# Kernel optimization log

Measured on AMD Instinct MI355X. Metric: run time of the kernel, lower is better.

The kernel has to match this reference:

```python
import jax, jax.numpy as jnp
import numpy as np

N = 50000      # nodes
E = 800000     # edges (before self-loops)
F = 128        # num_features
H = 64         # hidden_channels
B = 512        # batch_size (num graphs)
NC = 10        # num_classes


def setup_inputs() -> dict:
    key = jax.random.key(0)
    ks = jax.random.split(key, 24)
    rn = lambda k, shp, s=0.05: jax.random.normal(k, shp, jnp.float32) * s
    inp = {}
    inp["x"] = jax.random.normal(ks[0], (N, F), jnp.float32)
    inp["edge_index"] = jax.random.randint(ks[1], (2, E), 0, N)
    inp["batch"] = jnp.sort(jax.random.randint(ks[2], (N,), 0, B))
    # GATConv1: in F -> 4 heads x H (concat)
    inp["W1"] = rn(ks[3], (F, 4 * H)); inp["a_src1"] = rn(ks[4], (4, H))
    inp["a_dst1"] = rn(ks[5], (4, H)); inp["b1"] = rn(ks[6], (4 * H,))
    # GATConv2: in 4H -> 1 head x 2H
    inp["W2"] = rn(ks[7], (4 * H, 2 * H)); inp["a_src2"] = rn(ks[8], (1, 2 * H))
    inp["a_dst2"] = rn(ks[9], (1, 2 * H)); inp["b2"] = rn(ks[10], (2 * H,))
    # GCNConv: in 2H -> H
    inp["Wg"] = rn(ks[11], (2 * H, H)); inp["bg"] = rn(ks[12], (H,))
    # BatchNorms (eval mode: running_mean=0, running_var=1)
    inp["bn1_g"] = 1.0 + rn(ks[13], (4 * H,)); inp["bn1_b"] = rn(ks[14], (4 * H,))
    inp["bn2_g"] = 1.0 + rn(ks[15], (2 * H,)); inp["bn2_b"] = rn(ks[16], (2 * H,))
    inp["bn3_g"] = 1.0 + rn(ks[17], (2 * H,)); inp["bn3_b"] = rn(ks[18], (2 * H,))
    inp["lin1_W"] = rn(ks[19], (H, 128)); inp["lin1_b"] = rn(ks[20], (128,))
    inp["lin2_W"] = rn(ks[21], (128, NC)); inp["lin2_b"] = rn(ks[22], (NC,))
    inp["batch_size"] = B
    return inp


def _gat(x, src, dst, W, a_s, a_d, b, n):
    """PyG GATConv (eval): project, edge attention (leaky_relu 0.2), dst-softmax, scatter."""
    heads, ch = a_s.shape
    h = (x @ W).reshape(n, heads, ch)                       # [N, heads, ch]
    sc_s = (h * a_s).sum(-1)                                # [N, heads]
    sc_d = (h * a_d).sum(-1)
    e = jax.nn.leaky_relu(sc_s[src] + sc_d[dst], 0.2)       # [E2, heads]
    m = jax.ops.segment_max(e, dst, num_segments=n)
    ee = jnp.exp(e - m[dst])
    s = jax.ops.segment_sum(ee, dst, num_segments=n)
    alpha = ee / (s[dst] + 1e-16)                           # edge softmax per dst
    out = jax.ops.segment_sum(h[src] * alpha[:, :, None], dst, num_segments=n)
    return out.reshape(n, heads * ch) + b


def _bn_eval(x, g, b, eps=1e-5):
    # BatchNorm1d eval with running_mean=0, running_var=1
    return x * (g / jnp.sqrt(1.0 + eps)) + b


def reference(x, edge_index, batch, W1, a_src1, a_dst1, b1, W2, a_src2, a_dst2, b2,
              Wg, bg, bn1_g, bn1_b, bn2_g, bn2_b, bn3_g, bn3_b,
              lin1_W, lin1_b, lin2_W, lin2_b, batch_size):
    n = x.shape[0]
    loop = jnp.arange(n)
    src = jnp.concatenate([edge_index[0], loop])            # add self-loops (PyG default)
    dst = jnp.concatenate([edge_index[1], loop])
    lrelu = lambda v: jax.nn.leaky_relu(v, 0.01)            # module's LeakyReLU()

    x1 = _bn_eval(lrelu(_gat(x, src, dst, W1, a_src1, a_dst1, b1, n)), bn1_g, bn1_b)
    x2 = _bn_eval(lrelu(_gat(x1, src, dst, W2, a_src2, a_dst2, b2, n)), bn2_g, bn2_b)

    # GCNConv with symmetric normalization over A + I
    deg = jax.ops.segment_sum(jnp.ones_like(dst, jnp.float32), dst, num_segments=n)
    dis = jnp.where(deg > 0, jax.lax.rsqrt(deg), 0.0)
    h = x2 @ Wg                                             # [N, H]
    msg = h[src] * (dis[src] * dis[dst])[:, None]
    x3 = lrelu(jax.ops.segment_sum(msg, dst, num_segments=n) + bg)

    # global_mean_pool over graphs (dropout is identity in eval)
    sums = jax.ops.segment_sum(x3, batch, num_segments=batch_size)
    cnt = jax.ops.segment_sum(jnp.ones((n,), jnp.float32), batch, num_segments=batch_size)
    pooled = sums / jnp.clip(cnt, 1.0)[:, None]             # [B, H]

    y = lrelu(_bn_eval(pooled @ lin1_W + lin1_b, bn3_g, bn3_b))
    return y @ lin2_W + lin2_b                              # [B, NC]
```

## Files before the change

kernel.cpp:

```cpp
#include <hip/hip_runtime.h>
#include <hip/hip_bf16.h>

#define NN  50000
#define EE  800000
#define NE2 850000
#define NB  512
#define NRT 3125
#define NSB 196

#define BN_RS 0.9999950000374997f

typedef __attribute__((ext_vector_type(8))) short short8;
typedef __attribute__((ext_vector_type(4))) float f32x4;

__device__ __forceinline__ float bf2f(__hip_bfloat16 v) { return __bfloat162float(v); }
__device__ __forceinline__ unsigned short f2b(float v) {
    __hip_bfloat16 b = __float2bfloat16(v);
    return *reinterpret_cast<unsigned short*>(&b);
}
__device__ __forceinline__ float u2f(unsigned short u) {
    union { unsigned u; float f; } c; c.u = ((unsigned)u) << 16; return c.f;
}
__device__ __forceinline__ float4 u42f4(ushort4 v) {
    float4 r; r.x = u2f(v.x); r.y = u2f(v.y); r.z = u2f(v.z); r.w = u2f(v.w); return r;
}
__device__ __forceinline__ float lrelu01(float v) { return v > 0.f ? v : 0.01f * v; }
__device__ __forceinline__ float lrelu02(float v) { return v > 0.f ? v : 0.2f * v; }

__device__ __forceinline__ void up2(unsigned u, float& lo, float& hi) {
    union { unsigned x; float f; } a, b;
    a.x = u << 16; b.x = u & 0xFFFF0000u;
    lo = a.f; hi = b.f;
}
__device__ __forceinline__ void acc8(float* acc, uint4 u, float e) {
    float lo, hi;
    up2(u.x, lo, hi); acc[0] = fmaf(lo, e, acc[0]); acc[1] = fmaf(hi, e, acc[1]);
    up2(u.y, lo, hi); acc[2] = fmaf(lo, e, acc[2]); acc[3] = fmaf(hi, e, acc[3]);
    up2(u.z, lo, hi); acc[4] = fmaf(lo, e, acc[4]); acc[5] = fmaf(hi, e, acc[5]);
    up2(u.w, lo, hi); acc[6] = fmaf(lo, e, acc[6]); acc[7] = fmaf(hi, e, acc[7]);
}
__device__ __forceinline__ unsigned packbf2(float lo, float hi) {
    return ((unsigned)f2b(hi) << 16) | (unsigned)f2b(lo);
}

__device__ __forceinline__ void edge_sd(const int* __restrict__ ei, int e, int& s, int& d) {
    if (e < EE) { s = ei[e]; d = ei[EE + e]; }
    else        { s = e - EE; d = e - EE; }
}

__device__ __forceinline__ float ldf(const void* p, int i, bool bf) {
    return bf ? bf2f(((const __hip_bfloat16*)p)[i]) : ((const float*)p)[i];
}

#define NSEG 20
#define WTOT 85578
#define XQUADS (NN * 32)
#define PREP_TOT (XQUADS + WTOT + 32768 + 32768 + 8192 + NE2)
struct SegArgs { const void* src[NSEG]; int off[NSEG]; };

__global__ __launch_bounds__(256) void prep_k(SegArgs a,
                                              const void* __restrict__ x_raw,
                                              ushort4* __restrict__ xb4,
                                              const void* __restrict__ W1r,
                                              const void* __restrict__ W2r,
                                              const void* __restrict__ Wgr,
                                              float* __restrict__ wf,
                                              unsigned short* __restrict__ W1t,
                                              unsigned short* __restrict__ W2t,
                                              unsigned short* __restrict__ Wgt,
                                              const int* __restrict__ ei,
                                              int* __restrict__ degi,
                                              int* __restrict__ flag) {
    __shared__ int cnt;
    int t = threadIdx.x;
    if (t == 0) cnt = 0;
    __syncthreads();
    {
        int c = 0;
        const unsigned* xw = (const unsigned*)x_raw;
#pragma unroll
        for (int k = 0; k < 4; ++k) {
            unsigned w = xw[t * 4 + k];
            unsigned ef = (w >> 7) & 0xFFu;
            if (ef >= 100u && ef <= 140u) c++;
        }
        atomicAdd(&cnt, c);
    }
    __syncthreads();
    bool bf = (cnt > 512);
    if (blockIdx.x == 0 && t == 0) *flag = bf ? 1 : 0;

    int i = blockIdx.x * 256 + t;
    if (i >= PREP_TOT) return;
    if (i < XQUADS) {
        ushort4 o;
        if (bf) o = ((const ushort4*)x_raw)[i];
        else {
            float4 v = ((const float4*)x_raw)[i];
            o.x = f2b(v.x); o.y = f2b(v.y); o.z = f2b(v.z); o.w = f2b(v.w);
        }
        xb4[i] = o;
        return;
    }
    i -= XQUADS;
    if (i < WTOT) {
        int s = 0;
#pragma unroll
        for (int k = 1; k < NSEG; ++k) if (i >= a.off[k]) s = k;
        wf[i] = ldf(a.src[s], i - a.off[s], bf);
        return;
    }
    i -= WTOT;
    if (i < 32768) {
        int n = i >> 7, k = i & 127;
        W1t[i] = f2b(ldf(W1r, k * 256 + n, bf));
        return;
    }
    i -= 32768;
    if (i < 32768) {
        int n = i >> 8, k = i & 255;
        W2t[i] = f2b(ldf(W2r, k * 128 + n, bf));
        return;
    }
    i -= 32768;
    if (i < 8192) {
        int n = i >> 7, k = i & 127;
        Wgt[i] = f2b(ldf(Wgr, k * 64 + n, bf));
        return;
    }
    i -= 8192;
    {
        int s, d; edge_sd(ei, i, s, d);
        atomicAdd(&degi[d], 1);
    }
}

__global__ __launch_bounds__(256) void pscan_k(const int* __restrict__ degi,
                                               int* __restrict__ incl, int* __restrict__ bsum) {
    __shared__ int tmp[256];
    int t = threadIdx.x;
    int i = blockIdx.x * 256 + t;
    int v = (i < NN) ? degi[i] : 0;
    tmp[t] = v;
    __syncthreads();
#pragma unroll
    for (int off = 1; off < 256; off <<= 1) {
        int u = (t >= off) ? tmp[t - off] : 0;
        __syncthreads();
        tmp[t] += u;
        __syncthreads();
    }
    if (i < NN) incl[i] = tmp[t];
    if (t == 255) bsum[blockIdx.x] = tmp[255];
}

__global__ __launch_bounds__(256) void bscan_k(int* __restrict__ bsum) {
    __shared__ int tmp[256];
    int t = threadIdx.x;
    tmp[t] = (t < NSB) ? bsum[t] : 0;
    __syncthreads();
#pragma unroll
    for (int off = 1; off < 256; off <<= 1) {
        int u = (t >= off) ? tmp[t - off] : 0;
        __syncthreads();
        tmp[t] += u;
        __syncthreads();
    }
    if (t < NSB) bsum[t] = tmp[t];
}

__global__ __launch_bounds__(256) void fscan_k(const int* __restrict__ degi,
                                               const int* __restrict__ incl,
                                               const int* __restrict__ bsum,
                                               const int* __restrict__ batch,
                                               int* __restrict__ row_ptr, int* __restrict__ cursor,
                                               float* __restrict__ dis, int* __restrict__ gstart) {
    int i = blockIdx.x * 256 + threadIdx.x;
    if (i <= NB) {
        int lo = 0, hi = NN;
        while (lo < hi) { int mid = (lo + hi) >> 1; if (batch[mid] < i) lo = mid + 1; else hi = mid; }
        gstart[i] = lo;
    }
    if (i >= NN) return;
    int dg = degi[i];
    int base = (blockIdx.x > 0) ? bsum[blockIdx.x - 1] : 0;
    int ex = base + incl[i] - dg;
    row_ptr[i] = ex; cursor[i] = ex;
    dis[i] = dg > 0 ? rsqrtf((float)dg) : 0.f;
    if (i == NN - 1) row_ptr[NN] = bsum[NSB - 1];
}

__global__ __launch_bounds__(256) void scatter_k(const int* __restrict__ ei,
                                                 int* __restrict__ cursor,
                                                 int* __restrict__ csr_src) {
    int e = blockIdx.x * 256 + threadIdx.x;
    if (e >= NE2) return;
    int s, d; edge_sd(ei, e, s, d);
    int pos = atomicAdd(&cursor[d], 1);
    csr_src[pos] = s;
}

__global__ __launch_bounds__(256) void mgemm1_k(const short* __restrict__ A,
                                                const short* __restrict__ Bt,
                                                unsigned short* __restrict__ C,
                                                const float* __restrict__ a_s,
                                                const float* __restrict__ a_d,
                                                float* __restrict__ sc_s,
                                                float* __restrict__ sc_d) {
    int wave = threadIdx.x >> 6, lane = threadIdx.x & 63;
    int rt = blockIdx.x, cg = wave;
    int l15 = lane & 15, quad = lane >> 4;
    const short* ap = A + (size_t)(rt * 16 + l15) * 128 + quad * 8;
    const short* bp = Bt + (size_t)(cg * 64 + l15) * 128 + quad * 8;
    f32x4 acc[4] = {};
    for (int k0 = 0; k0 < 128; k0 += 32) {
        short8 a = *(const short8*)(ap + k0);
#pragma unroll
        for (int j = 0; j < 4; ++j) {
            short8 b = *(const short8*)(bp + (size_t)j * 16 * 128 + k0);
            acc[j] = __builtin_amdgcn_mfma_f32_16x16x32_bf16(a, b, acc[j], 0, 0, 0);
        }
    }
    float asv[4], adv[4];
#pragma unroll
    for (int j = 0; j < 4; ++j) {
        asv[j] = a_s[cg * 64 + j * 16 + l15];
        adv[j] = a_d[cg * 64 + j * 16 + l15];
    }
    float ss[4] = {0.f, 0.f, 0.f, 0.f}, sd[4] = {0.f, 0.f, 0.f, 0.f};
#pragma unroll
    for (int j = 0; j < 4; ++j) {
        int n = cg * 64 + j * 16 + l15;
#pragma unroll
        for (int r = 0; r < 4; ++r) {
            float v = acc[j][r];
            C[(size_t)(rt * 16 + quad * 4 + r) * 256 + n] = f2b(v);
            ss[r] = fmaf(v, asv[j], ss[r]);
            sd[r] = fmaf(v, adv[j], sd[r]);
        }
    }
#pragma unroll
    for (int off = 1; off < 16; off <<= 1) {
#pragma unroll
        for (int r = 0; r < 4; ++r) {
            ss[r] += __shfl_xor(ss[r], off);
            sd[r] += __shfl_xor(sd[r], off);
        }
    }
    if (l15 == 0) {
#pragma unroll
        for (int r = 0; r < 4; ++r) {
            int node = rt * 16 + quad * 4 + r;
            sc_s[node * 4 + cg] = ss[r];
            sc_d[node * 4 + cg] = sd[r];
        }
    }
}

__global__ __launch_bounds__(256) void mgemm2_k(const short* __restrict__ A,
                                                const short* __restrict__ Bt,
                                                unsigned short* __restrict__ C,
                                                const float* __restrict__ a_s,
                                                const float* __restrict__ a_d,
                                                float* __restrict__ sc_s,
                                                float* __restrict__ sc_d) {
    __shared__ float sred[4][16][2];
    int wave = threadIdx.x >> 6, lane = threadIdx.x & 63;
    int gidx = blockIdx.x * 4 + wave;
    bool act = gidx < NRT * 2;
    int gcl = act ? gidx : NRT * 2 - 1;
    int rt = gcl >> 1, cg = gcl & 1;
    int l15 = lane & 15, quad = lane >> 4;
    const short* ap = A + (size_t)(rt * 16 + l15) * 256 + quad * 8;
    const short* bp = Bt + (size_t)(cg * 64 + l15) * 256 + quad * 8;
    f32x4 acc[4] = {};
    for (int k0 = 0; k0 < 256; k0 += 32) {
        short8 a = *(const short8*)(ap + k0);
#pragma unroll
        for (int j = 0; j < 4; ++j) {
            short8 b = *(const short8*)(bp + (size_t)j * 16 * 256 + k0);
            acc[j] = __builtin_amdgcn_mfma_f32_16x16x32_bf16(a, b, acc[j], 0, 0, 0);
        }
    }
    float asv[4], adv[4];
#pragma unroll
    for (int j = 0; j < 4; ++j) {
        asv[j] = a_s[cg * 64 + j * 16 + l15];
        adv[j] = a_d[cg * 64 + j * 16 + l15];
    }
    float ss[4] = {0.f, 0.f, 0.f, 0.f}, sd[4] = {0.f, 0.f, 0.f, 0.f};
#pragma unroll
    for (int j = 0; j < 4; ++j) {
        int n = cg * 64 + j * 16 + l15;
#pragma unroll
        for (int r = 0; r < 4; ++r) {
            float v = acc[j][r];
            if (act) C[(size_t)(rt * 16 + quad * 4 + r) * 128 + n] = f2b(v);
            ss[r] = fmaf(v, asv[j], ss[r]);
            sd[r] = fmaf(v, adv[j], sd[r]);
        }
    }
#pragma unroll
    for (int off = 1; off < 16; off <<= 1) {
#pragma unroll
        for (int r = 0; r < 4; ++r) {
            ss[r] += __shfl_xor(ss[r], off);
            sd[r] += __shfl_xor(sd[r], off);
        }
    }
    if (l15 == 0) {
#pragma unroll
        for (int r = 0; r < 4; ++r) {
            sred[wave][quad * 4 + r][0] = ss[r];
            sred[wave][quad * 4 + r][1] = sd[r];
        }
    }
    __syncthreads();
    if (threadIdx.x < 32) {
        int rl = threadIdx.x >> 4, row = threadIdx.x & 15;
        int g2 = blockIdx.x * 4 + rl * 2;
        if (g2 < NRT * 2) {
            int node = (g2 >> 1) * 16 + row;
            sc_s[node] = sred[rl * 2][row][0] + sred[rl * 2 + 1][row][0];
            sc_d[node] = sred[rl * 2][row][1] + sred[rl * 2 + 1][row][1];
        }
    }
}

__global__ __launch_bounds__(256) void mgemm3_k(const short* __restrict__ A,
                                                const short* __restrict__ Bt,
                                                unsigned short* __restrict__ C) {
    int wave = threadIdx.x >> 6, lane = threadIdx.x & 63;
    int gidx = blockIdx.x * 4 + wave;
    if (gidx >= NRT) return;
    int rt = gidx;
    int l15 = lane & 15, quad = lane >> 4;
    const short* ap = A + (size_t)(rt * 16 + l15) * 128 + quad * 8;
    const short* bp = Bt + (size_t)l15 * 128 + quad * 8;
    f32x4 acc[4] = {};
    for (int k0 = 0; k0 < 128; k0 += 32) {
        short8 a = *(const short8*)(ap + k0);
#pragma unroll
        for (int j = 0; j < 4; ++j) {
            short8 b = *(const short8*)(bp + (size_t)j * 16 * 128 + k0);
            acc[j] = __builtin_amdgcn_mfma_f32_16x16x32_bf16(a, b, acc[j], 0, 0, 0);
        }
    }
#pragma unroll
    for (int j = 0; j < 4; ++j) {
        int n = j * 16 + l15;
#pragma unroll
        for (int r = 0; r < 4; ++r)
            C[(size_t)(rt * 16 + quad * 4 + r) * 64 + n] = f2b(acc[j][r]);
    }
}

__device__ __forceinline__ float sel4(float4 v, int head) {
    float ab = (head & 1) ? v.y : v.x;
    float cd = (head & 1) ? v.w : v.z;
    return (head & 2) ? cd : ab;
}

__global__ __launch_bounds__(256) void agg1_k(const int* __restrict__ row_ptr,
                                              const int* __restrict__ csr_src,
                                              const uint4* __restrict__ h1b,
                                              const float4* __restrict__ sc_s4,
                                              const float4* __restrict__ sc_d4,
                                              const float4* __restrict__ b1,
                                              const float4* __restrict__ g1,
                                              const float4* __restrict__ bb1,
                                              uint4* __restrict__ x1b) {
    int n = __builtin_amdgcn_readfirstlane((blockIdx.x * 256 + threadIdx.x) >> 6);
    int lane = threadIdx.x & 63;
    if (n >= NN) return;
    int g = lane >> 5, sl = lane & 31;
    int head = sl >> 3;
    int row = row_ptr[n], end = row_ptr[n + 1];
    float scd_h = sel4(sc_d4[n], head);
    float acc[8] = {0.f, 0.f, 0.f, 0.f, 0.f, 0.f, 0.f, 0.f};
    float den = 0.f;
    int c = row + g;
    for (; c + 6 < end; c += 8) {
        int s0 = csr_src[c], s1 = csr_src[c + 2], s2 = csr_src[c + 4], s3 = csr_src[c + 6];
        float4 q0 = sc_s4[s0], q1 = sc_s4[s1], q2 = sc_s4[s2], q3 = sc_s4[s3];
        uint4 u0 = h1b[(size_t)s0 * 32 + sl];
        uint4 u1 = h1b[(size_t)s1 * 32 + sl];
        uint4 u2 = h1b[(size_t)s2 * 32 + sl];
        uint4 u3 = h1b[(size_t)s3 * 32 + sl];
        float e0 = __expf(lrelu02(sel4(q0, head) + scd_h));
        float e1 = __expf(lrelu02(sel4(q1, head) + scd_h));
        float e2 = __expf(lrelu02(sel4(q2, head) + scd_h));
        float e3 = __expf(lrelu02(sel4(q3, head) + scd_h));
        den += (e0 + e1) + (e2 + e3);
        acc8(acc, u0, e0); acc8(acc, u1, e1); acc8(acc, u2, e2); acc8(acc, u3, e3);
    }
    for (; c < end; c += 2) {
        int s0 = csr_src[c];
        float4 q0 = sc_s4[s0];
        uint4 u0 = h1b[(size_t)s0 * 32 + sl];
        float e0 = __expf(lrelu02(sel4(q0, head) + scd_h));
        den += e0;
        acc8(acc, u0, e0);
    }
    den += __shfl_xor(den, 32);
#pragma unroll
    for (int k = 0; k < 8; ++k) acc[k] += __shfl_xor(acc[k], 32);
    if (g == 0) {
        float inv = 1.f / (den + 1e-16f);
        float4 bA = b1[sl * 2],  bB = b1[sl * 2 + 1];
        float4 gA = g1[sl * 2],  gB = g1[sl * 2 + 1];
        float4 eA = bb1[sl * 2], eB = bb1[sl * 2 + 1];
        float o0 = lrelu01(fmaf(acc[0], inv, bA.x)) * (gA.x * BN_RS) + eA.x;
        float o1 = lrelu01(fmaf(acc[1], inv, bA.y)) * (gA.y * BN_RS) + eA.y;
        float o2 = lrelu01(fmaf(acc[2], inv, bA.z)) * (gA.z * BN_RS) + eA.z;
        float o3 = lrelu01(fmaf(acc[3], inv, bA.w)) * (gA.w * BN_RS) + eA.w;
        float o4 = lrelu01(fmaf(acc[4], inv, bB.x)) * (gB.x * BN_RS) + eB.x;
        float o5 = lrelu01(fmaf(acc[5], inv, bB.y)) * (gB.y * BN_RS) + eB.y;
        float o6 = lrelu01(fmaf(acc[6], inv, bB.z)) * (gB.z * BN_RS) + eB.z;
        float o7 = lrelu01(fmaf(acc[7], inv, bB.w)) * (gB.w * BN_RS) + eB.w;
        uint4 w;
        w.x = packbf2(o0, o1); w.y = packbf2(o2, o3);
        w.z = packbf2(o4, o5); w.w = packbf2(o6, o7);
        x1b[(size_t)n * 32 + sl] = w;
    }
}

__global__ __launch_bounds__(256) void agg2_k(const int* __restrict__ row_ptr,
                                              const int* __restrict__ csr_src,
                                              const uint4* __restrict__ h2b,
                                              const float* __restrict__ sc_s,
                                              const float* __restrict__ sc_d,
                                              const float4* __restrict__ b2,
                                              const float4* __restrict__ g2,
                                              const float4* __restrict__ bb2,
                                              uint4* __restrict__ x2b) {
    int n = __builtin_amdgcn_readfirstlane((blockIdx.x * 256 + threadIdx.x) >> 6);
    int lane = threadIdx.x & 63;
    if (n >= NN) return;
    int g = lane >> 4, sl = lane & 15;
    int row = row_ptr[n], end = row_ptr[n + 1];
    float scd = sc_d[n];
    float acc[8] = {0.f, 0.f, 0.f, 0.f, 0.f, 0.f, 0.f, 0.f};
    float den = 0.f;
    int c = row + g;
    for (; c + 12 < end; c += 16) {
        int s0 = csr_src[c], s1 = csr_src[c + 4], s2 = csr_src[c + 8], s3 = csr_src[c + 12];
        float c0 = sc_s[s0], c1 = sc_s[s1], c2 = sc_s[s2], c3 = sc_s[s3];
        uint4 u0 = h2b[(size_t)s0 * 16 + sl];
        uint4 u1 = h2b[(size_t)s1 * 16 + sl];
        uint4 u2 = h2b[(size_t)s2 * 16 + sl];
        uint4 u3 = h2b[(size_t)s3 * 16 + sl];
        float e0 = __expf(lrelu02(c0 + scd));
        float e1 = __expf(lrelu02(c1 + scd));
        float e2 = __expf(lrelu02(c2 + scd));
        float e3 = __expf(lrelu02(c3 + scd));
        den += (e0 + e1) + (e2 + e3);
        acc8(acc, u0, e0); acc8(acc, u1, e1); acc8(acc, u2, e2); acc8(acc, u3, e3);
    }
    for (; c < end; c += 4) {
        int s0 = csr_src[c];
        float e0 = __expf(lrelu02(sc_s[s0] + scd));
        uint4 u0 = h2b[(size_t)s0 * 16 + sl];
        den += e0;
        acc8(acc, u0, e0);
    }
    den += __shfl_xor(den, 16);
    den += __shfl_xor(den, 32);
#pragma unroll
    for (int k = 0; k < 8; ++k) {
        acc[k] += __shfl_xor(acc[k], 16);
        acc[k] += __shfl_xor(acc[k], 32);
    }
    if (lane < 16) {
        float inv = 1.f / (den + 1e-16f);
        float4 bA = b2[sl * 2],  bB = b2[sl * 2 + 1];
        float4 gA = g2[sl * 2],  gB = g2[sl * 2 + 1];
        float4 eA = bb2[sl * 2], eB = bb2[sl * 2 + 1];
        float o0 = lrelu01(fmaf(acc[0], inv, bA.x)) * (gA.x * BN_RS) + eA.x;
        float o1 = lrelu01(fmaf(acc[1], inv, bA.y)) * (gA.y * BN_RS) + eA.y;
        float o2 = lrelu01(fmaf(acc[2], inv, bA.z)) * (gA.z * BN_RS) + eA.z;
        float o3 = lrelu01(fmaf(acc[3], inv, bA.w)) * (gA.w * BN_RS) + eA.w;
        float o4 = lrelu01(fmaf(acc[4], inv, bB.x)) * (gB.x * BN_RS) + eB.x;
        float o5 = lrelu01(fmaf(acc[5], inv, bB.y)) * (gB.y * BN_RS) + eB.y;
        float o6 = lrelu01(fmaf(acc[6], inv, bB.z)) * (gB.z * BN_RS) + eB.z;
        float o7 = lrelu01(fmaf(acc[7], inv, bB.w)) * (gB.w * BN_RS) + eB.w;
        uint4 w;
        w.x = packbf2(o0, o1); w.y = packbf2(o2, o3);
        w.z = packbf2(o4, o5); w.w = packbf2(o6, o7);
        x2b[(size_t)n * 16 + sl] = w;
    }
}

__global__ __launch_bounds__(256) void gcn_k(const int* __restrict__ row_ptr,
                                             const int* __restrict__ csr_src,
                                             const uint4* __restrict__ hgb,
                                             const float* __restrict__ dis,
                                             const float4* __restrict__ bg,
                                             float4* __restrict__ x3) {
    int n = __builtin_amdgcn_readfirstlane((blockIdx.x * 256 + threadIdx.x) >> 6);
    int lane = threadIdx.x & 63;
    if (n >= NN) return;
    int g = lane >> 3, sl = lane & 7;
    int row = row_ptr[n], end = row_ptr[n + 1];
    float dn = dis[n];
    float acc[8] = {0.f, 0.f, 0.f, 0.f, 0.f, 0.f, 0.f, 0.f};
    int c = row + g;
    for (; c + 8 < end; c += 16) {
        int s0 = csr_src[c], s1 = csr_src[c + 8];
        float w0 = dis[s0], w1 = dis[s1];
        uint4 u0 = hgb[(size_t)s0 * 8 + sl];
        uint4 u1 = hgb[(size_t)s1 * 8 + sl];
        acc8(acc, u0, w0); acc8(acc, u1, w1);
    }
    for (; c < end; c += 8) {
        int s0 = csr_src[c];
        float w0 = dis[s0];
        uint4 u0 = hgb[(size_t)s0 * 8 + sl];
        acc8(acc, u0, w0);
    }
#pragma unroll
    for (int off = 8; off <= 32; off <<= 1) {
#pragma unroll
        for (int k = 0; k < 8; ++k) acc[k] += __shfl_xor(acc[k], off);
    }
    if (lane < 8) {
        float4 bA = bg[sl * 2], bB = bg[sl * 2 + 1];
        float4 oA, oB;
        oA.x = lrelu01(fmaf(acc[0], dn, bA.x));
        oA.y = lrelu01(fmaf(acc[1], dn, bA.y));
        oA.z = lrelu01(fmaf(acc[2], dn, bA.z));
        oA.w = lrelu01(fmaf(acc[3], dn, bA.w));
        oB.x = lrelu01(fmaf(acc[4], dn, bB.x));
        oB.y = lrelu01(fmaf(acc[5], dn, bB.y));
        oB.z = lrelu01(fmaf(acc[6], dn, bB.z));
        oB.w = lrelu01(fmaf(acc[7], dn, bB.w));
        x3[(size_t)n * 16 + sl * 2]     = oA;
        x3[(size_t)n * 16 + sl * 2 + 1] = oB;
    }
}

__global__ __launch_bounds__(256) void poolmlp_k(const float* __restrict__ x3,
                                                 const int* __restrict__ gstart,
                                                 const float* __restrict__ l1W,
                                                 const float* __restrict__ l1b,
                                                 const float* __restrict__ g3,
                                                 const float* __restrict__ b3,
                                                 const float* __restrict__ l2W,
                                                 const float* __restrict__ l2b,
                                                 void* __restrict__ outp,
                                                 const int* __restrict__ flag) {
    __shared__ float red[4][64];
    __shared__ float pl[64];
    __shared__ float y1s[128];
    int g = blockIdx.x, t = threadIdx.x;
    int c = t & 63, r = t >> 6;
    int s = gstart[g], e = gstart[g + 1];
    float sum = 0.f;
    for (int n = s + r; n < e; n += 4) sum += x3[(size_t)n * 64 + c];
    red[r][c] = sum;
    __syncthreads();
    if (t < 64) {
        float v = red[0][t] + red[1][t] + red[2][t] + red[3][t];
        int cnt = e - s; if (cnt < 1) cnt = 1;
        pl[t] = v / (float)cnt;
    }
    __syncthreads();
    if (t < 128) {
        float acc = l1b[t];
#pragma unroll 8
        for (int j = 0; j < 64; ++j) acc = fmaf(pl[j], l1W[j * 128 + t], acc);
        acc = acc * (g3[t] * BN_RS) + b3[t];
        y1s[t] = lrelu01(acc);
    }
    __syncthreads();
    if (t < 10) {
        float o = l2b[t];
#pragma unroll 8
        for (int j = 0; j < 128; ++j) o = fmaf(y1s[j], l2W[j * 10 + t], o);
        if (*flag) ((__hip_bfloat16*)outp)[g * 10 + t] = __float2bfloat16(o);
        else       ((float*)outp)[g * 10 + t] = o;
    }
}

static const int kSegN[NSEG]  = {32768, 256, 256, 256, 32768, 128, 128, 128, 8192, 64,
                                 256, 256, 128, 128, 128, 128, 8192, 128, 1280, 10};
static const int kSegIn[NSEG] = {3, 4, 5, 6, 7, 8, 9, 10, 11, 12, 13, 14, 15, 16, 17, 18, 19, 20, 21, 22};

extern "C" void kernel_launch(void* const* d_in, const int* in_sizes, int n_in,
                              void* d_out, int out_size, void* d_ws, size_t ws_size,
                              hipStream_t stream) {
    const void* x_raw = d_in[0];
    const int*  ei    = (const int*)d_in[1];
    const int*  batch = (const int*)d_in[2];

    int*   flag = (int*)d_ws;
    float* ws   = (float*)d_ws;
    unsigned short* xb = (unsigned short*)(ws + 16);
    float* wf   = ws + 16 + (size_t)NN * 64;
    unsigned short* W1t = (unsigned short*)(wf + 85584);
    unsigned short* W2t = W1t + 32768;
    unsigned short* Wgt = W2t + 32768;
    unsigned short* h1b = Wgt + 8192;
    unsigned short* x1b = h1b + (size_t)NN * 256;
    unsigned short* x2b = x1b + (size_t)NN * 256;
    unsigned short* hgb = x2b + (size_t)NN * 128;
    float* x3   = (float*)(hgb + (size_t)NN * 64);
    float* sc_s1 = x3 + (size_t)NN * 64;
    float* sc_d1 = sc_s1 + (size_t)NN * 4;
    float* sc_s2 = sc_d1 + (size_t)NN * 4;
    float* sc_d2 = sc_s2 + NN;
    float* disb  = sc_d2 + NN;
    int*   gstart = (int*)(disb + NN);
    int*   degi   = gstart + NB + 4;
    int*   incl   = degi + NN;
    int*   bsum   = incl + NN;
    int*   row_ptr = bsum + 256;
    int*   cursor  = row_ptr + NN + 1;
    int*   csr_src = cursor + NN;

    int off[NSEG]; int o = 0;
    for (int s = 0; s < NSEG; ++s) { off[s] = o; o += kSegN[s]; }
    float* as1f = wf + off[1];  float* ad1f = wf + off[2];
    float* b1f  = wf + off[3];  float* as2f = wf + off[5];
    float* ad2f = wf + off[6];  float* b2f  = wf + off[7];
    float* bgf  = wf + off[9];  float* bn1g = wf + off[10]; float* bn1b = wf + off[11];
    float* bn2g = wf + off[12]; float* bn2b = wf + off[13]; float* bn3g = wf + off[14];
    float* bn3b = wf + off[15]; float* l1Wf = wf + off[16]; float* l1bf = wf + off[17];
    float* l2Wf = wf + off[18]; float* l2bf = wf + off[19];

    unsigned short* h2b = h1b;

    hipMemsetAsync(degi, 0, NN * sizeof(int), stream);
    SegArgs sa;
    for (int s = 0; s < NSEG; ++s) { sa.src[s] = d_in[kSegIn[s]]; sa.off[s] = off[s]; }
    prep_k<<<(PREP_TOT + 255) / 256, 256, 0, stream>>>(sa, x_raw, (ushort4*)xb,
                                                       d_in[3], d_in[7], d_in[11],
                                                       wf, W1t, W2t, Wgt, ei, degi, flag);

    pscan_k<<<NSB, 256, 0, stream>>>(degi, incl, bsum);
    bscan_k<<<1, 256, 0, stream>>>(bsum);
    fscan_k<<<NSB, 256, 0, stream>>>(degi, incl, bsum, batch, row_ptr, cursor, disb, gstart);
    scatter_k<<<(NE2 + 255) / 256, 256, 0, stream>>>(ei, cursor, csr_src);

    mgemm1_k<<<NRT, 256, 0, stream>>>((const short*)xb, (const short*)W1t, h1b,
                                      as1f, ad1f, sc_s1, sc_d1);
    agg1_k<<<12500, 256, 0, stream>>>(row_ptr, csr_src, (const uint4*)h1b,
                                      (const float4*)sc_s1, (const float4*)sc_d1,
                                      (const float4*)b1f, (const float4*)bn1g,
                                      (const float4*)bn1b, (uint4*)x1b);

    mgemm2_k<<<(NRT * 2 + 3) / 4, 256, 0, stream>>>((const short*)x1b, (const short*)W2t, h2b,
                                                    as2f, ad2f, sc_s2, sc_d2);
    agg2_k<<<12500, 256, 0, stream>>>(row_ptr, csr_src, (const uint4*)h2b,
                                      sc_s2, sc_d2,
                                      (const float4*)b2f, (const float4*)bn2g,
                                      (const float4*)bn2b, (uint4*)x2b);

    mgemm3_k<<<(NRT + 3) / 4, 256, 0, stream>>>((const short*)x2b, (const short*)Wgt, hgb);
    gcn_k<<<12500, 256, 0, stream>>>(row_ptr, csr_src, (const uint4*)hgb, disb,
                                     (const float4*)bgf, (float4*)x3);
    poolmlp_k<<<NB, 256, 0, stream>>>(x3, gstart, l1Wf, l1bf, bn3g, bn3b, l2Wf, l2bf,
                                      d_out, flag);
}
```

Measured before the change: 445.8 us.

## Precompute per-edge attention exponentials and GCN weights in CSR order before aggregation

Adds a csr_dst array and two edge-parallel kernels that compute the exp(leaky_relu) attention weights for both GAT layers and the GCN normalisation weight per CSR edge. The aggregation kernels then read these contiguous per-edge values instead of gathering source scores and recomputing exponentials. This swaps random gathers of sc_s and dis for streamed edge arrays, at the cost of two extra launches and extra global traffic. The scratch buffers alias x2b, xb and x3, which depends on those buffers not being live at the time.

```diff
diff --git a/kernel.cpp b/kernel.cpp
--- a/kernel.cpp
+++ b/kernel.cpp
@@ -7,6 +7,7 @@
 #define NB  512
 #define NRT 3125
 #define NSB 196
+#define NEB ((NE2 + 255) / 256)
 
 #define BN_RS 0.9999950000374997f
 
@@ -192,12 +193,45 @@
 
 __global__ __launch_bounds__(256) void scatter_k(const int* __restrict__ ei,
                                                  int* __restrict__ cursor,
-                                                 int* __restrict__ csr_src) {
+                                                 int* __restrict__ csr_src,
+                                                 int* __restrict__ csr_dst) {
     int e = blockIdx.x * 256 + threadIdx.x;
     if (e >= NE2) return;
     int s, d; edge_sd(ei, e, s, d);
     int pos = atomicAdd(&cursor[d], 1);
     csr_src[pos] = s;
+    csr_dst[pos] = d;
+}
+
+__global__ __launch_bounds__(256) void escore1_k(const int* __restrict__ csr_src,
+                                                 const int* __restrict__ csr_dst,
+                                                 const float4* __restrict__ sc_s4,
+                                                 const float4* __restrict__ sc_d4,
+                                                 float4* __restrict__ ce1) {
+    int p = blockIdx.x * 256 + threadIdx.x;
+    if (p >= NE2) return;
+    int s = csr_src[p], d = csr_dst[p];
+    float4 a = sc_s4[s], b = sc_d4[d];
+    float4 o;
+    o.x = __expf(lrelu02(a.x + b.x));
+    o.y = __expf(lrelu02(a.y + b.y));
+    o.z = __expf(lrelu02(a.z + b.z));
+    o.w = __expf(lrelu02(a.w + b.w));
+    ce1[p] = o;
+}
+
+__global__ __launch_bounds__(256) void escore2_k(const int* __restrict__ csr_src,
+                                                 const int* __restrict__ csr_dst,
+                                                 const float* __restrict__ sc_s,
+                                                 const float* __restrict__ sc_d,
+                                                 const float* __restrict__ dis,
+                                                 float* __restrict__ ce2,
+                                                 float* __restrict__ cwg) {
+    int p = blockIdx.x * 256 + threadIdx.x;
+    if (p >= NE2) return;
+    int s = csr_src[p], d = csr_dst[p];
+    ce2[p] = __expf(lrelu02(sc_s[s] + sc_d[d]));
+    cwg[p] = dis[s] * dis[d];
 }
 
 __global__ __launch_bounds__(256) void mgemm1_k(const short* __restrict__ A,
@@ -355,17 +389,10 @@
     }
 }
 
-__device__ __forceinline__ float sel4(float4 v, int head) {
-    float ab = (head & 1) ? v.y : v.x;
-    float cd = (head & 1) ? v.w : v.z;
-    return (head & 2) ? cd : ab;
-}
-
 __global__ __launch_bounds__(256) void agg1_k(const int* __restrict__ row_ptr,
                                               const int* __restrict__ csr_src,
                                               const uint4* __restrict__ h1b,
-                                              const float4* __restrict__ sc_s4,
-                                              const float4* __restrict__ sc_d4,
+                                              const float* __restrict__ ce1,
                                               const float4* __restrict__ b1,
                                               const float4* __restrict__ g1,
                                               const float4* __restrict__ bb1,
@@ -376,29 +403,25 @@
     int g = lane >> 5, sl = lane & 31;
     int head = sl >> 3;
     int row = row_ptr[n], end = row_ptr[n + 1];
-    float scd_h = sel4(sc_d4[n], head);
     float acc[8] = {0.f, 0.f, 0.f, 0.f, 0.f, 0.f, 0.f, 0.f};
     float den = 0.f;
-    int c = row + g;
-    for (; c + 6 < end; c += 8) {
-        int s0 = csr_src[c], s1 = csr_src[c + 2], s2 = csr_src[c + 4], s3 = csr_src[c + 6];
-        float4 q0 = sc_s4[s0], q1 = sc_s4[s1], q2 = sc_s4[s2], q3 = sc_s4[s3];
+    int c = row;
+    for (; c + 7 < end; c += 8) {
+        int i0 = c + g, i1 = c + 2 + g, i2 = c + 4 + g, i3 = c + 6 + g;
+        float e0 = ce1[i0 * 4 + head], e1 = ce1[i1 * 4 + head];
+        float e2 = ce1[i2 * 4 + head], e3 = ce1[i3 * 4 + head];
+        int s0 = csr_src[i0], s1 = csr_src[i1], s2 = csr_src[i2], s3 = csr_src[i3];
         uint4 u0 = h1b[(size_t)s0 * 32 + sl];
         uint4 u1 = h1b[(size_t)s1 * 32 + sl];
         uint4 u2 = h1b[(size_t)s2 * 32 + sl];
         uint4 u3 = h1b[(size_t)s3 * 32 + sl];
-        float e0 = __expf(lrelu02(sel4(q0, head) + scd_h));
-        float e1 = __expf(lrelu02(sel4(q1, head) + scd_h));
-        float e2 = __expf(lrelu02(sel4(q2, head) + scd_h));
-        float e3 = __expf(lrelu02(sel4(q3, head) + scd_h));
         den += (e0 + e1) + (e2 + e3);
         acc8(acc, u0, e0); acc8(acc, u1, e1); acc8(acc, u2, e2); acc8(acc, u3, e3);
     }
-    for (; c < end; c += 2) {
-        int s0 = csr_src[c];
-        float4 q0 = sc_s4[s0];
+    for (int cg2 = c + g; cg2 < end; cg2 += 2) {
+        float e0 = ce1[cg2 * 4 + head];
+        int s0 = csr_src[cg2];
         uint4 u0 = h1b[(size_t)s0 * 32 + sl];
-        float e0 = __expf(lrelu02(sel4(q0, head) + scd_h));
         den += e0;
         acc8(acc, u0, e0);
     }
@@ -428,8 +451,7 @@
 __global__ __launch_bounds__(256) void agg2_k(const int* __restrict__ row_ptr,
                                               const int* __restrict__ csr_src,
                                               const uint4* __restrict__ h2b,
-                                              const float* __restrict__ sc_s,
-                                              const float* __restrict__ sc_d,
+                                              const float* __restrict__ ce2,
                                               const float4* __restrict__ b2,
                                               const float4* __restrict__ g2,
                                               const float4* __restrict__ bb2,
@@ -439,27 +461,22 @@
     if (n >= NN) return;
     int g = lane >> 4, sl = lane & 15;
     int row = row_ptr[n], end = row_ptr[n + 1];
-    float scd = sc_d[n];
     float acc[8] = {0.f, 0.f, 0.f, 0.f, 0.f, 0.f, 0.f, 0.f};
     float den = 0.f;
     int c = row + g;
     for (; c + 12 < end; c += 16) {
         int s0 = csr_src[c], s1 = csr_src[c + 4], s2 = csr_src[c + 8], s3 = csr_src[c + 12];
-        float c0 = sc_s[s0], c1 = sc_s[s1], c2 = sc_s[s2], c3 = sc_s[s3];
+        float e0 = ce2[c], e1 = ce2[c + 4], e2 = ce2[c + 8], e3 = ce2[c + 12];
         uint4 u0 = h2b[(size_t)s0 * 16 + sl];
         uint4 u1 = h2b[(size_t)s1 * 16 + sl];
         uint4 u2 = h2b[(size_t)s2 * 16 + sl];
         uint4 u3 = h2b[(size_t)s3 * 16 + sl];
-        float e0 = __expf(lrelu02(c0 + scd));
-        float e1 = __expf(lrelu02(c1 + scd));
-        float e2 = __expf(lrelu02(c2 + scd));
-        float e3 = __expf(lrelu02(c3 + scd));
         den += (e0 + e1) + (e2 + e3);
         acc8(acc, u0, e0); acc8(acc, u1, e1); acc8(acc, u2, e2); acc8(acc, u3, e3);
     }
     for (; c < end; c += 4) {
         int s0 = csr_src[c];
-        float e0 = __expf(lrelu02(sc_s[s0] + scd));
+        float e0 = ce2[c];
         uint4 u0 = h2b[(size_t)s0 * 16 + sl];
         den += e0;
         acc8(acc, u0, e0);
@@ -494,7 +511,7 @@
 __global__ __launch_bounds__(256) void gcn_k(const int* __restrict__ row_ptr,
                                              const int* __restrict__ csr_src,
                                              const uint4* __restrict__ hgb,
-                                             const float* __restrict__ dis,
+                                             const float* __restrict__ cwg,
                                              const float4* __restrict__ bg,
                                              float4* __restrict__ x3) {
     int n = __builtin_amdgcn_readfirstlane((blockIdx.x * 256 + threadIdx.x) >> 6);
@@ -502,19 +519,18 @@
     if (n >= NN) return;
     int g = lane >> 3, sl = lane & 7;
     int row = row_ptr[n], end = row_ptr[n + 1];
-    float dn = dis[n];
     float acc[8] = {0.f, 0.f, 0.f, 0.f, 0.f, 0.f, 0.f, 0.f};
     int c = row + g;
     for (; c + 8 < end; c += 16) {
         int s0 = csr_src[c], s1 = csr_src[c + 8];
-        float w0 = dis[s0], w1 = dis[s1];
+        float w0 = cwg[c], w1 = cwg[c + 8];
         uint4 u0 = hgb[(size_t)s0 * 8 + sl];
         uint4 u1 = hgb[(size_t)s1 * 8 + sl];
         acc8(acc, u0, w0); acc8(acc, u1, w1);
     }
     for (; c < end; c += 8) {
         int s0 = csr_src[c];
-        float w0 = dis[s0];
+        float w0 = cwg[c];
         uint4 u0 = hgb[(size_t)s0 * 8 + sl];
         acc8(acc, u0, w0);
     }
@@ -526,14 +542,14 @@
     if (lane < 8) {
         float4 bA = bg[sl * 2], bB = bg[sl * 2 + 1];
         float4 oA, oB;
-        oA.x = lrelu01(fmaf(acc[0], dn, bA.x));
-        oA.y = lrelu01(fmaf(acc[1], dn, bA.y));
-        oA.z = lrelu01(fmaf(acc[2], dn, bA.z));
-        oA.w = lrelu01(fmaf(acc[3], dn, bA.w));
-        oB.x = lrelu01(fmaf(acc[4], dn, bB.x));
-        oB.y = lrelu01(fmaf(acc[5], dn, bB.y));
-        oB.z = lrelu01(fmaf(acc[6], dn, bB.z));
-        oB.w = lrelu01(fmaf(acc[7], dn, bB.w));
+        oA.x = lrelu01(acc[0] + bA.x);
+        oA.y = lrelu01(acc[1] + bA.y);
+        oA.z = lrelu01(acc[2] + bA.z);
+        oA.w = lrelu01(acc[3] + bA.w);
+        oB.x = lrelu01(acc[4] + bB.x);
+        oB.y = lrelu01(acc[5] + bB.y);
+        oB.z = lrelu01(acc[6] + bB.z);
+        oB.w = lrelu01(acc[7] + bB.w);
         x3[(size_t)n * 16 + sl * 2]     = oA;
         x3[(size_t)n * 16 + sl * 2 + 1] = oB;
     }
@@ -618,6 +634,11 @@
     int*   cursor  = row_ptr + NN + 1;
     int*   csr_src = cursor + NN;
 
+    int*   csr_dst = (int*)x3;
+    float* ce1 = (float*)x2b;
+    float* ce2 = (float*)xb;
+    float* cwg = ((float*)xb) + 1048576;
+
     int off[NSEG]; int o = 0;
     for (int s = 0; s < NSEG; ++s) { off[s] = o; o += kSegN[s]; }
     float* as1f = wf + off[1];  float* ad1f = wf + off[2];
@@ -640,24 +661,26 @@
     pscan_k<<<NSB, 256, 0, stream>>>(degi, incl, bsum);
     bscan_k<<<1, 256, 0, stream>>>(bsum);
     fscan_k<<<NSB, 256, 0, stream>>>(degi, incl, bsum, batch, row_ptr, cursor, disb, gstart);
-    scatter_k<<<(NE2 + 255) / 256, 256, 0, stream>>>(ei, cursor, csr_src);
+    scatter_k<<<NEB, 256, 0, stream>>>(ei, cursor, csr_src, csr_dst);
 
     mgemm1_k<<<NRT, 256, 0, stream>>>((const short*)xb, (const short*)W1t, h1b,
                                       as1f, ad1f, sc_s1, sc_d1);
-    agg1_k<<<12500, 256, 0, stream>>>(row_ptr, csr_src, (const uint4*)h1b,
-                                      (const float4*)sc_s1, (const float4*)sc_d1,
+    escore1_k<<<NEB, 256, 0, stream>>>(csr_src, csr_dst,
+                                       (const float4*)sc_s1, (const float4*)sc_d1,
+                                       (float4*)ce1);
+    agg1_k<<<12500, 256, 0, stream>>>(row_ptr, csr_src, (const uint4*)h1b, ce1,
                                       (const float4*)b1f, (const float4*)bn1g,
                                       (const float4*)bn1b, (uint4*)x1b);
 
     mgemm2_k<<<(NRT * 2 + 3) / 4, 256, 0, stream>>>((const short*)x1b, (const short*)W2t, h2b,
                                                     as2f, ad2f, sc_s2, sc_d2);
-    agg2_k<<<12500, 256, 0, stream>>>(row_ptr, csr_src, (const uint4*)h2b,
-                                      sc_s2, sc_d2,
+    escore2_k<<<NEB, 256, 0, stream>>>(csr_src, csr_dst, sc_s2, sc_d2, disb, ce2, cwg);
+    agg2_k<<<12500, 256, 0, stream>>>(row_ptr, csr_src, (const uint4*)h2b, ce2,
                                       (const float4*)b2f, (const float4*)bn2g,
                                       (const float4*)bn2b, (uint4*)x2b);
 
     mgemm3_k<<<(NRT + 3) / 4, 256, 0, stream>>>((const short*)x2b, (const short*)Wgt, hgb);
-    gcn_k<<<12500, 256, 0, stream>>>(row_ptr, csr_src, (const uint4*)hgb, disb,
+    gcn_k<<<12500, 256, 0, stream>>>(row_ptr, csr_src, (const uint4*)hgb, cwg,
                                      (const float4*)bgf, (float4*)x3);
     poolmlp_k<<<NB, 256, 0, stream>>>(x3, gstart, l1Wf, l1bf, bn3g, bn3b, l2Wf, l2bf,
                                       d_out, flag);
```

Measured after the change: 449.8 us. About the same (+0.9%).
